# Optimization experiments

Measured on AMD Instinct MI355X. Metric: run time of the kernel, lower is better.

The kernel has to match this reference:

```python
import jax, jax.numpy as jnp
import numpy as np

V, E, H, C_TAGS, B, T = 32000, 256, 200, 20, 64, 512
LN_EPS = 1e-5


def setup_inputs() -> dict:
    key = jax.random.key(0)
    ks = jax.random.split(key, 12)
    s = 0.05
    return {
        "words": jax.random.randint(ks[0], (B, T), 0, V),
        "seq_len": jax.random.randint(ks[1], (B,), T // 2, T + 1),
        "target": jax.random.randint(ks[2], (B, T), 0, C_TAGS),
        "embed_table": jax.random.normal(ks[3], (V, E)) * s,
        "ln_gamma": jnp.ones((E,)),
        "ln_beta": jnp.zeros((E,)),
        "w_ih_f": jax.random.normal(ks[4], (4 * H, E)) * s,
        "w_hh_f": jax.random.normal(ks[5], (4 * H, H)) * s,
        "b_f": jnp.zeros((4 * H,)),  # b_ih + b_hh folded together
        "w_ih_b": jax.random.normal(ks[6], (4 * H, E)) * s,
        "w_hh_b": jax.random.normal(ks[7], (4 * H, H)) * s,
        "b_b": jnp.zeros((4 * H,)),
        "fc_w": jax.random.normal(ks[8], (C_TAGS, 2 * H)) * s,
        "fc_b": jnp.zeros((C_TAGS,)),
        "trans": jax.random.normal(ks[9], (C_TAGS, C_TAGS)) * s,
        "start_scores": jax.random.normal(ks[10], (C_TAGS,)) * s,
        "end_scores": jax.random.normal(ks[11], (C_TAGS,)) * s,
    }


def _lstm_dir(x, m, w_ih, w_hh, b, reverse):
    """x: [T,B,E] time-major, m: [T,B] float mask. Packed-sequence semantics:
    carry only updates on valid steps (matters for the reverse direction)."""
    Hn = w_hh.shape[1]
    gates_x = jnp.einsum('tbe,ge->tbg', x, w_ih) + b  # [T,B,4H], batched GEMM

    def step(carry, xs):
        h, c = carry
        gx, mt = xs
        g = gx + h @ w_hh.T
        i, f, gg, o = jnp.split(g, 4, axis=-1)  # torch gate order i,f,g,o
        c_new = jax.nn.sigmoid(f) * c + jax.nn.sigmoid(i) * jnp.tanh(gg)
        h_new = jax.nn.sigmoid(o) * jnp.tanh(c_new)
        mt = mt[:, None]
        h = mt * h_new + (1.0 - mt) * h
        c = mt * c_new + (1.0 - mt) * c
        return (h, c), h

    init = (jnp.zeros((x.shape[1], Hn), x.dtype), jnp.zeros((x.shape[1], Hn), x.dtype))
    _, hs = jax.lax.scan(step, init, (gates_x, m), reverse=reverse)
    return hs  # [T,B,H]


def _crf_nll(logits, mask, target, trans, start, end):
    """Linear-chain CRF NLL with start/end transitions. logits [B,T,C] (emissions),
    mask [B,T] float, target [B,T] int. Returns per-sample loss [B]."""
    # --- log partition via forward algorithm (scan over time) ---
    alpha0 = start[None, :] + logits[:, 0]  # [B,C]
    emits = jnp.swapaxes(logits, 0, 1)[1:]  # [T-1,B,C]
    ms = jnp.swapaxes(mask, 0, 1)[1:]       # [T-1,B]

    def step(alpha, xs):
        emit, mt = xs
        scores = alpha[:, :, None] + trans[None, :, :] + emit[:, None, :]  # [B,C,C]
        new = jax.nn.logsumexp(scores, axis=1)
        alpha = jnp.where(mt[:, None] > 0, new, alpha)
        return alpha, None

    alpha, _ = jax.lax.scan(step, alpha0, (emits, ms))
    logZ = jax.nn.logsumexp(alpha + end[None, :], axis=1)  # [B]

    # --- gold path score ---
    emit_gold = jnp.take_along_axis(logits, target[..., None], axis=2)[..., 0]  # [B,T]
    emit_score = jnp.sum(emit_gold * mask, axis=1)
    trans_gold = trans[target[:, :-1], target[:, 1:]]  # [B,T-1]
    trans_score = jnp.sum(trans_gold * mask[:, 1:], axis=1)
    last_idx = jnp.sum(mask, axis=1).astype(jnp.int32) - 1
    last_tag = jnp.take_along_axis(target, last_idx[:, None], axis=1)[:, 0]
    gold = emit_score + trans_score + start[target[:, 0]] + end[last_tag]
    return logZ - gold


def reference(words, seq_len, target, embed_table, ln_gamma, ln_beta,
              w_ih_f, w_hh_f, b_f, w_ih_b, w_hh_b, b_b,
              fc_w, fc_b, trans, start_scores, end_scores):
    # Embedding + LayerNorm
    x = embed_table[words]  # [B,T,E]
    mu = x.mean(-1, keepdims=True)
    var = ((x - mu) ** 2).mean(-1, keepdims=True)
    x = (x - mu) * jax.lax.rsqrt(var + LN_EPS) * ln_gamma + ln_beta

    mask = (jnp.arange(x.shape[1])[None, :] < seq_len[:, None]).astype(x.dtype)  # [B,T]
    xt = jnp.swapaxes(x, 0, 1)       # [T,B,E]
    mt = jnp.swapaxes(mask, 0, 1)    # [T,B]

    # BiLSTM (num_layers=1)
    hf = _lstm_dir(xt, mt, w_ih_f, w_hh_f, b_f, reverse=False)
    hb = _lstm_dir(xt, mt, w_ih_b, w_hh_b, b_b, reverse=True)
    feats = jnp.swapaxes(jnp.concatenate([hf, hb], axis=-1), 0, 1)  # [B,T,2H]

    # fc + dropout (eval: identity) + log_softmax emissions
    feats = feats @ fc_w.T + fc_b
    logits = jax.nn.log_softmax(feats, axis=-1)

    loss = _crf_nll(logits, mask, target, trans, start_scores, end_scores)
    return loss.mean()
```

## Files before the change

### kernel.cpp

```cpp
#include <hip/hip_runtime.h>

#define TT 512
#define BB 64
#define EE 256
#define HH 200
#define GG 800
#define CC 20
#define MM (BB * TT)

typedef _Float16 f16x8 __attribute__((ext_vector_type(8)));
typedef float    f32x4 __attribute__((ext_vector_type(4)));
typedef _Float16 f16x2 __attribute__((ext_vector_type(2)));

#if __has_builtin(__builtin_amdgcn_mfma_f32_16x16x32_f16)
#define HAVE_MFMA_F16 1
#else
#define HAVE_MFMA_F16 0
#endif

__device__ __forceinline__ float bf2f(unsigned short u) {
  return __uint_as_float(((unsigned int)u) << 16);
}
__device__ __forceinline__ unsigned short f2bf(float f) {
  unsigned int u = __float_as_uint(f);
  return (unsigned short)((u + 0x7fffu + ((u >> 16) & 1u)) >> 16);
}
__device__ __forceinline__ float sigf(float x) { return 1.0f / (1.0f + __expf(-x)); }
__device__ __forceinline__ float tanhfast(float x) {
  return 1.0f - 2.0f / (__expf(2.0f * x) + 1.0f);
}
union U32H2 { unsigned int u; f16x2 h; };
__device__ __forceinline__ unsigned int bfpair_to_h2bits(unsigned int p) {
  U32H2 r;
  r.h[0] = (_Float16)bf2f((unsigned short)(p & 0xffffu));
  r.h[1] = (_Float16)bf2f((unsigned short)(p >> 16));
  return r.u;
}
__device__ __forceinline__ float dot2acc(f16x2 a, f16x2 b, float c) {
#if __has_builtin(__builtin_amdgcn_fdot2)
  return __builtin_amdgcn_fdot2(a, b, c, false);
#else
  return c + (float)a[0] * (float)b[0] + (float)a[1] * (float)b[1];
#endif
}

#define NSEG 14
struct CvtArgs { const void* src[NSEG]; };
__constant__ const int cvt_cum[NSEG + 1] = {
    0, 8192000, 8192256, 8192512, 8397312, 8557312, 8558112,
    8762912, 8922912, 8923712, 8931712, 8931732, 8932132, 8932152, 8932172};

__global__ __launch_bounds__(256) void k_convert(CvtArgs a,
                                                 unsigned short* __restrict__ dst) {
  const bool f32mode = (((const unsigned int*)a.src[1])[0] == 0x3F800000u);
  int gi0 = (blockIdx.x * 256 + threadIdx.x) * 4;
#pragma unroll
  for (int r = 0; r < 4; ++r) {
    int gi = gi0 + r;
    if (gi >= cvt_cum[NSEG]) return;
    int seg = 0;
#pragma unroll
    for (int s = 1; s < NSEG; ++s) seg += (gi >= cvt_cum[s]) ? 1 : 0;
    int local = gi - cvt_cum[seg];
    unsigned short v;
    if (f32mode) v = f2bf(((const float*)a.src[seg])[local]);
    else         v = ((const unsigned short*)a.src[seg])[local];
    dst[gi] = v;
  }
}

__global__ __launch_bounds__(256) void k_embed_ln(
    const int* __restrict__ words, const unsigned short* __restrict__ etab,
    const unsigned short* __restrict__ gamma, const unsigned short* __restrict__ beta,
    unsigned short* __restrict__ x) {
  int m = blockIdx.x;
  int e = threadIdx.x;
  int w = words[m];
  float v = bf2f(etab[(size_t)w * EE + e]);
  float s = v, ss = v * v;
#pragma unroll
  for (int off = 32; off > 0; off >>= 1) {
    s += __shfl_xor(s, off, 64);
    ss += __shfl_xor(ss, off, 64);
  }
  __shared__ float red[2][4];
  int wv = e >> 6;
  if ((e & 63) == 0) { red[0][wv] = s; red[1][wv] = ss; }
  __syncthreads();
  float S = red[0][0] + red[0][1] + red[0][2] + red[0][3];
  float SS = red[1][0] + red[1][1] + red[1][2] + red[1][3];
  float mu = S * (1.0f / EE);
  float var = fmaxf(SS * (1.0f / EE) - mu * mu, 0.0f);
  float nrm = (v - mu) * rsqrtf(var + 1e-5f) * bf2f(gamma[e]) + bf2f(beta[e]);
  x[(size_t)m * EE + e] = f2bf(nrm);
}

#if HAVE_MFMA_F16
__global__ __launch_bounds__(256) void k_gates(
    const unsigned short* __restrict__ x,
    const unsigned short* __restrict__ wih_f, const unsigned short* __restrict__ wih_b,
    const unsigned short* __restrict__ bias_f, const unsigned short* __restrict__ bias_b,
    unsigned short* __restrict__ gates) {
  const int dir = blockIdx.z;
  const unsigned short* wih = dir ? wih_b : wih_f;
  const unsigned short* bias = dir ? bias_b : bias_f;
  const int m0 = blockIdx.x * 64;
  const int n0 = blockIdx.y * 64;
  __shared__ __align__(16) _Float16 As[64 * 32];
  __shared__ __align__(16) _Float16 Bs[64 * 32];
  const int tid = threadIdx.x;
  const int lane = tid & 63, wave = tid >> 6;
  const int wm = (wave >> 1) * 32, wn = (wave & 1) * 32;
  const int srow = tid >> 2, sq = tid & 3;
  const int mrow = lane & 15, q = lane >> 4;
  f32x4 acc[2][2] = {};
  for (int kk = 0; kk < EE; kk += 32) {
    union { int4 v; unsigned short u[8]; } ua, ub;
    ua.v = *(const int4*)(x + (size_t)(m0 + srow) * EE + kk + sq * 8);
    ub.v.x = 0; ub.v.y = 0; ub.v.z = 0; ub.v.w = 0;
    int n = n0 + srow;
    if (n < GG) ub.v = *(const int4*)(wih + (size_t)n * EE + kk + sq * 8);
    f16x8 af, bf;
#pragma unroll
    for (int r = 0; r < 8; ++r) {
      af[r] = (_Float16)bf2f(ua.u[r]);
      bf[r] = (_Float16)bf2f(ub.u[r]);
    }
    __syncthreads();
    *(f16x8*)(As + srow * 32 + sq * 8) = af;
    *(f16x8*)(Bs + srow * 32 + sq * 8) = bf;
    __syncthreads();
    f16x8 a0 = *(const f16x8*)(As + (wm + mrow) * 32 + q * 8);
    f16x8 a1 = *(const f16x8*)(As + (wm + 16 + mrow) * 32 + q * 8);
    f16x8 b0 = *(const f16x8*)(Bs + (wn + mrow) * 32 + q * 8);
    f16x8 b1 = *(const f16x8*)(Bs + (wn + 16 + mrow) * 32 + q * 8);
    acc[0][0] = __builtin_amdgcn_mfma_f32_16x16x32_f16(a0, b0, acc[0][0], 0, 0, 0);
    acc[0][1] = __builtin_amdgcn_mfma_f32_16x16x32_f16(a0, b1, acc[0][1], 0, 0, 0);
    acc[1][0] = __builtin_amdgcn_mfma_f32_16x16x32_f16(a1, b0, acc[1][0], 0, 0, 0);
    acc[1][1] = __builtin_amdgcn_mfma_f32_16x16x32_f16(a1, b1, acc[1][1], 0, 0, 0);
  }
#pragma unroll
  for (int im = 0; im < 2; ++im) {
#pragma unroll
    for (int in = 0; in < 2; ++in) {
      int n = n0 + wn + in * 16 + mrow;
      if (n < GG) {
        float bb = bf2f(bias[n]);
#pragma unroll
        for (int r = 0; r < 4; ++r) {
          int mg = m0 + wm + im * 16 + q * 4 + r;
          gates[((size_t)dir * MM + mg) * GG + n] = f2bf(acc[im][in][r] + bb);
        }
      }
    }
  }
}
#else
__global__ __launch_bounds__(256) void k_gates(
    const unsigned short* __restrict__ x,
    const unsigned short* __restrict__ wih_f, const unsigned short* __restrict__ wih_b,
    const unsigned short* __restrict__ bias_f, const unsigned short* __restrict__ bias_b,
    unsigned short* __restrict__ gates) {
  const int dir = blockIdx.z;
  const unsigned short* wih = dir ? wih_b : wih_f;
  const unsigned short* bias = dir ? bias_b : bias_f;
  const int m0 = blockIdx.x * 64;
  const int n0 = blockIdx.y * 64;
  for (int r = 0; r < 16; ++r) {
    int idx = threadIdx.x + 256 * r;
    int m = m0 + (idx >> 6), n = n0 + (idx & 63);
    if (n >= GG) continue;
    float acc = bf2f(bias[n]);
    const unsigned short* xr = x + (size_t)m * EE;
    const unsigned short* wr = wih + (size_t)n * EE;
    for (int k = 0; k < EE; ++k) acc += bf2f(xr[k]) * bf2f(wr[k]);
    gates[((size_t)dir * MM + m) * GG + n] = f2bf(acc);
  }
}
#endif

__global__ __launch_bounds__(832)
__attribute__((amdgpu_waves_per_eu(4, 4)))
void k_lstm(
    const unsigned short* __restrict__ gates,
    const unsigned short* __restrict__ whh_f, const unsigned short* __restrict__ whh_b,
    const int* __restrict__ seq_len,
    unsigned short* __restrict__ h_out) {
  const int b = blockIdx.x & (BB - 1);
  const int dir = blockIdx.x >> 6;
  const unsigned short* whh = dir ? whh_b : whh_f;
  const int tid = threadIdx.x;
  const int L = seq_len[b];
  __shared__ __align__(16) _Float16 hsh[HH];
  __shared__ float gbuf[GG];
  unsigned int w2u[100];
  if (tid < GG) {
    const unsigned short* wr = whh + (size_t)tid * HH;
#pragma unroll
    for (int i = 0; i < 25; ++i) {
      int4 wvv = *(const int4*)(wr + i * 8);
      w2u[4 * i + 0] = bfpair_to_h2bits((unsigned int)wvv.x);
      w2u[4 * i + 1] = bfpair_to_h2bits((unsigned int)wvv.y);
      w2u[4 * i + 2] = bfpair_to_h2bits((unsigned int)wvv.z);
      w2u[4 * i + 3] = bfpair_to_h2bits((unsigned int)wvv.w);
      asm volatile("" : "+v"(w2u[4 * i + 0]), "+v"(w2u[4 * i + 1]),
                        "+v"(w2u[4 * i + 2]), "+v"(w2u[4 * i + 3]));
    }
  }
  if (tid < HH) hsh[tid] = (_Float16)0.0f;
  float c_st = 0.0f, h_st = 0.0f;
  const unsigned short* gbase = gates + ((size_t)dir * MM + (size_t)b * TT) * GG + tid;
  unsigned short* hobase = h_out + (size_t)(dir * BB + b) * TT * HH;
  float gx_cur = 0.0f;
  if (tid < GG) {
    int t0 = dir ? (TT - 1) : 0;
    gx_cur = bf2f(gbase[(size_t)t0 * GG]);
  }
  __syncthreads();
  for (int s = 0; s < TT; ++s) {
    const int t = dir ? (TT - 1 - s) : s;
    if (tid < GG) {
      int sn = (s + 1 < TT) ? (s + 1) : s;
      int tn = dir ? (TT - 1 - sn) : sn;
      float gx_next = bf2f(gbase[(size_t)tn * GG]);
      float acc0 = gx_cur, acc1 = 0.0f;
#pragma unroll
      for (int g = 0; g < 7; ++g) {
        const int nk = (g < 6) ? 4 : 1;
        union { int4 v; f16x2 h[4]; } u[4];
#pragma unroll
        for (int k = 0; k < 4; ++k)
          if (k < nk) u[k].v = *(const int4*)(hsh + (g * 4 + k) * 8);
#pragma unroll
        for (int k = 0; k < 4; ++k) {
          if (k < nk) {
            const int i = g * 4 + k;
            U32H2 w0, w1, w2, w3;
            w0.u = w2u[4 * i + 0]; w1.u = w2u[4 * i + 1];
            w2.u = w2u[4 * i + 2]; w3.u = w2u[4 * i + 3];
            acc0 = dot2acc(w0.h, u[k].h[0], acc0);
            acc1 = dot2acc(w1.h, u[k].h[1], acc1);
            acc0 = dot2acc(w2.h, u[k].h[2], acc0);
            acc1 = dot2acc(w3.h, u[k].h[3], acc1);
          }
        }
#if __has_builtin(__builtin_amdgcn_sched_barrier)
        __builtin_amdgcn_sched_barrier(0);
#endif
      }
      gbuf[tid] = acc0 + acc1;
      gx_cur = gx_next;
    }
    __syncthreads();
    if (tid < HH) {
      float gi = gbuf[tid], gf = gbuf[HH + tid];
      float gg = gbuf[2 * HH + tid], go = gbuf[3 * HH + tid];
      float cn = sigf(gf) * c_st + sigf(gi) * tanhfast(gg);
      float hn = sigf(go) * tanhfast(cn);
      if (t < L) { c_st = cn; h_st = hn; }
      hsh[tid] = (_Float16)h_st;
      hobase[(size_t)t * HH + tid] = f2bf(h_st);
    }
    __syncthreads();
  }
}

__global__ __launch_bounds__(256) void k_fc(
    const unsigned short* __restrict__ h_out,
    const unsigned short* __restrict__ fc_w, const unsigned short* __restrict__ fc_b,
    float* __restrict__ logits) {
  __shared__ __align__(16) unsigned short hsh[4][2 * HH];
  const int wv = threadIdx.x >> 6, lane = threadIdx.x & 63;
  const int m = blockIdx.x * 4 + wv;
  if (lane < 25) {
    *(int4*)&hsh[wv][lane * 8] = *(const int4*)(h_out + (size_t)m * HH + lane * 8);
  } else if (lane < 50) {
    *(int4*)&hsh[wv][HH + (lane - 25) * 8] =
        *(const int4*)(h_out + (size_t)MM * HH + (size_t)m * HH + (lane - 25) * 8);
  }
  __syncthreads();
  float s = -3.0e38f;
  if (lane < CC) {
    s = bf2f(fc_b[lane]);
    const unsigned short* wrow = fc_w + lane * 2 * HH;
    for (int jj = 0; jj < 50; ++jj) {
      union { int4 v; unsigned short u[8]; } hw, ww;
      hw.v = *(const int4*)&hsh[wv][jj * 8];
      ww.v = *(const int4*)(wrow + jj * 8);
#pragma unroll
      for (int r = 0; r < 8; ++r) s += bf2f(hw.u[r]) * bf2f(ww.u[r]);
    }
  }
  float mx = s;
#pragma unroll
  for (int off = 32; off > 0; off >>= 1) mx = fmaxf(mx, __shfl_xor(mx, off, 64));
  float ex = (lane < CC) ? __expf(s - mx) : 0.0f;
  float sm = ex;
#pragma unroll
  for (int off = 32; off > 0; off >>= 1) sm += __shfl_xor(sm, off, 64);
  if (lane < CC) logits[(size_t)m * CC + lane] = s - mx - __logf(sm);
}

__global__ __launch_bounds__(64) void k_crf(
    const float* __restrict__ logits, const int* __restrict__ target,
    const int* __restrict__ seq_len, const unsigned short* __restrict__ trans,
    const unsigned short* __restrict__ startv, const unsigned short* __restrict__ endv,
    float* __restrict__ loss_b) {
  const int b = blockIdx.x, lane = threadIdx.x;
  const int L = seq_len[b];
  const int* tg = target + b * TT;
  const float* lg = logits + (size_t)b * TT * CC;
  float tcol[CC];
#pragma unroll
  for (int i = 0; i < CC; ++i) tcol[i] = (lane < CC) ? bf2f(trans[i * CC + lane]) : 0.0f;
  float g = 0.0f;
  for (int t = lane; t < TT; t += 64) {
    if (t < L) {
      g += lg[t * CC + tg[t]];
      if (t >= 1) g += bf2f(trans[tg[t - 1] * CC + tg[t]]);
    }
  }
#pragma unroll
  for (int off = 32; off > 0; off >>= 1) g += __shfl_xor(g, off, 64);
  float alpha = (lane < CC) ? (bf2f(startv[lane]) + lg[lane]) : -3.0e38f;
  for (int t = 1; t < L; ++t) {
    float e = (lane < CC) ? lg[t * CC + lane] : 0.0f;
    float sc[CC];
#pragma unroll
    for (int i = 0; i < CC; ++i) sc[i] = __shfl(alpha, i, 64) + tcol[i];
    float mx = sc[0];
#pragma unroll
    for (int i = 1; i < CC; ++i) mx = fmaxf(mx, sc[i]);
    float sm = 0.0f;
#pragma unroll
    for (int i = 0; i < CC; ++i) sm += __expf(sc[i] - mx);
    float na = mx + __logf(sm) + e;
    if (lane < CC) alpha = na;
  }
  float v = (lane < CC) ? (alpha + bf2f(endv[lane])) : -3.0e38f;
  float mx = v;
#pragma unroll
  for (int off = 32; off > 0; off >>= 1) mx = fmaxf(mx, __shfl_xor(mx, off, 64));
  float ex = (lane < CC) ? __expf(v - mx) : 0.0f;
#pragma unroll
  for (int off = 32; off > 0; off >>= 1) ex += __shfl_xor(ex, off, 64);
  if (lane == 0) {
    float logZ = mx + __logf(ex);
    float gold = g + bf2f(startv[tg[0]]) + bf2f(endv[tg[L - 1]]);
    loss_b[b] = logZ - gold;
  }
}

__global__ __launch_bounds__(64) void k_mean(const float* __restrict__ loss_b,
                                             unsigned int* __restrict__ out) {
  float v = loss_b[threadIdx.x];
#pragma unroll
  for (int off = 32; off > 0; off >>= 1) v += __shfl_xor(v, off, 64);
  if (threadIdx.x == 0) {
    float mean = v * (1.0f / BB);
    unsigned int lo = (unsigned int)f2bf(mean);
    unsigned int hi = __float_as_uint(mean) >> 16;
    out[0] = (hi << 16) | lo;
  }
}

extern "C" void kernel_launch(void* const* d_in, const int* in_sizes, int n_in,
                              void* d_out, int out_size, void* d_ws, size_t ws_size,
                              hipStream_t stream) {
  const int* words   = (const int*)d_in[0];
  const int* seq_len = (const int*)d_in[1];
  const int* target  = (const int*)d_in[2];

  char* ws = (char*)d_ws;
  const size_t x_off      = 0;
  const size_t gates_off  = x_off + 16777216;
  const size_t h_off      = gates_off + 104857600;
  const size_t logits_off = h_off + 26214400;
  const size_t loss_off   = logits_off + 2621440;
  const size_t cvt_off    = loss_off + 256;
  unsigned short* x      = (unsigned short*)(ws + x_off);
  unsigned short* gatesb = (unsigned short*)(ws + gates_off);
  unsigned short* h_out  = (unsigned short*)(ws + h_off);
  float* logits          = (float*)(ws + logits_off);
  float* loss_b          = (float*)(ws + loss_off);
  unsigned short* wcvt   = (unsigned short*)(ws + cvt_off);

  unsigned short* etab_c  = wcvt + 0;
  unsigned short* gamma_c = wcvt + 8192000;
  unsigned short* beta_c  = wcvt + 8192256;
  unsigned short* wih_f_c = wcvt + 8192512;
  unsigned short* whh_f_c = wcvt + 8397312;
  unsigned short* b_f_c   = wcvt + 8557312;
  unsigned short* wih_b_c = wcvt + 8558112;
  unsigned short* whh_b_c = wcvt + 8762912;
  unsigned short* b_b_c   = wcvt + 8922912;
  unsigned short* fc_w_c  = wcvt + 8923712;
  unsigned short* fc_b_c  = wcvt + 8931712;
  unsigned short* trans_c = wcvt + 8931732;
  unsigned short* start_c = wcvt + 8932132;
  unsigned short* end_c   = wcvt + 8932152;

  CvtArgs ca;
  for (int i = 0; i < NSEG; ++i) ca.src[i] = d_in[3 + i];
  const int total_cvt = 8932172;
  k_convert<<<(total_cvt + 1023) / 1024, 256, 0, stream>>>(ca, wcvt);

  k_embed_ln<<<MM, 256, 0, stream>>>(words, etab_c, gamma_c, beta_c, x);
  k_gates<<<dim3(MM / 64, 13, 2), 256, 0, stream>>>(x, wih_f_c, wih_b_c, b_f_c, b_b_c, gatesb);
  k_lstm<<<128, 832, 0, stream>>>(gatesb, whh_f_c, whh_b_c, seq_len, h_out);
  k_fc<<<MM / 4, 256, 0, stream>>>(h_out, fc_w_c, fc_b_c, logits);
  k_crf<<<BB, 64, 0, stream>>>(logits, target, seq_len, trans_c, start_c, end_c, loss_b);
  k_mean<<<1, 64, 0, stream>>>(loss_b, (unsigned int*)d_out);
}
```

Before: 1.199 ms.

## Compute all four gates per thread in LSTM recurrence, double-buffer hidden state

The recurrent LSTM kernel now runs one thread per hidden unit instead of one thread per gate row. Each thread holds the four gate rows of W_hh in registers (400 packed half2 words) and computes the gate pre-activations and the cell update itself. This removes the shared gate buffer and one of the two barriers per timestep. The hidden state in shared memory is double-buffered to avoid a read/write race. The cost is serial work per thread growing about fourfold, and a very large register footprint at one wave per EU, which risks spilling and lower latency hiding.

```diff
diff --git a/kernel.cpp b/kernel.cpp
--- a/kernel.cpp
+++ b/kernel.cpp
@@ -179,8 +179,8 @@
 }
 #endif
 
-__global__ __launch_bounds__(832)
-__attribute__((amdgpu_waves_per_eu(4, 4)))
+__global__ __launch_bounds__(256)
+__attribute__((amdgpu_waves_per_eu(1, 1)))
 void k_lstm(
     const unsigned short* __restrict__ gates,
     const unsigned short* __restrict__ whh_f, const unsigned short* __restrict__ whh_b,
@@ -191,75 +191,81 @@
   const unsigned short* whh = dir ? whh_b : whh_f;
   const int tid = threadIdx.x;
   const int L = seq_len[b];
-  __shared__ __align__(16) _Float16 hsh[HH];
-  __shared__ float gbuf[GG];
-  unsigned int w2u[100];
-  if (tid < GG) {
-    const unsigned short* wr = whh + (size_t)tid * HH;
-#pragma unroll
-    for (int i = 0; i < 25; ++i) {
-      int4 wvv = *(const int4*)(wr + i * 8);
-      w2u[4 * i + 0] = bfpair_to_h2bits((unsigned int)wvv.x);
-      w2u[4 * i + 1] = bfpair_to_h2bits((unsigned int)wvv.y);
-      w2u[4 * i + 2] = bfpair_to_h2bits((unsigned int)wvv.z);
-      w2u[4 * i + 3] = bfpair_to_h2bits((unsigned int)wvv.w);
-      asm volatile("" : "+v"(w2u[4 * i + 0]), "+v"(w2u[4 * i + 1]),
-                        "+v"(w2u[4 * i + 2]), "+v"(w2u[4 * i + 3]));
-    }
-  }
-  if (tid < HH) hsh[tid] = (_Float16)0.0f;
+  __shared__ __align__(16) _Float16 hsh[2][HH];
+  unsigned int w2u[400];
+  if (tid < HH) {
+#pragma unroll
+    for (int r = 0; r < 4; ++r) {
+      const unsigned short* wr = whh + (size_t)(tid + r * HH) * HH;
+#pragma unroll
+      for (int i = 0; i < 25; ++i) {
+        int4 wv = *(const int4*)(wr + i * 8);
+        const int base = r * 100 + i * 4;
+        w2u[base + 0] = bfpair_to_h2bits((unsigned int)wv.x);
+        w2u[base + 1] = bfpair_to_h2bits((unsigned int)wv.y);
+        w2u[base + 2] = bfpair_to_h2bits((unsigned int)wv.z);
+        w2u[base + 3] = bfpair_to_h2bits((unsigned int)wv.w);
+        asm volatile("" : "+v"(w2u[base + 0]), "+v"(w2u[base + 1]),
+                          "+v"(w2u[base + 2]), "+v"(w2u[base + 3]));
+      }
+    }
+    hsh[0][tid] = (_Float16)0.0f;
+  }
   float c_st = 0.0f, h_st = 0.0f;
-  const unsigned short* gbase = gates + ((size_t)dir * MM + (size_t)b * TT) * GG + tid;
+  const unsigned short* gbase = gates + ((size_t)dir * MM + (size_t)b * TT) * GG;
   unsigned short* hobase = h_out + (size_t)(dir * BB + b) * TT * HH;
-  float gx_cur = 0.0f;
-  if (tid < GG) {
-    int t0 = dir ? (TT - 1) : 0;
-    gx_cur = bf2f(gbase[(size_t)t0 * GG]);
+  float gx0 = 0, gx1 = 0, gx2 = 0, gx3 = 0;
+  if (tid < HH) {
+    const int t0 = dir ? (TT - 1) : 0;
+    gx0 = bf2f(gbase[(size_t)t0 * GG + tid]);
+    gx1 = bf2f(gbase[(size_t)t0 * GG + tid + HH]);
+    gx2 = bf2f(gbase[(size_t)t0 * GG + tid + 2 * HH]);
+    gx3 = bf2f(gbase[(size_t)t0 * GG + tid + 3 * HH]);
   }
   __syncthreads();
   for (int s = 0; s < TT; ++s) {
     const int t = dir ? (TT - 1 - s) : s;
-    if (tid < GG) {
-      int sn = (s + 1 < TT) ? (s + 1) : s;
-      int tn = dir ? (TT - 1 - sn) : sn;
-      float gx_next = bf2f(gbase[(size_t)tn * GG]);
-      float acc0 = gx_cur, acc1 = 0.0f;
-#pragma unroll
-      for (int g = 0; g < 7; ++g) {
-        const int nk = (g < 6) ? 4 : 1;
-        union { int4 v; f16x2 h[4]; } u[4];
-#pragma unroll
-        for (int k = 0; k < 4; ++k)
-          if (k < nk) u[k].v = *(const int4*)(hsh + (g * 4 + k) * 8);
-#pragma unroll
-        for (int k = 0; k < 4; ++k) {
-          if (k < nk) {
-            const int i = g * 4 + k;
+    const int p = s & 1;
+    if (tid < HH) {
+      const int sn = (s + 1 < TT) ? (s + 1) : s;
+      const int tn = dir ? (TT - 1 - sn) : sn;
+      float n0 = bf2f(gbase[(size_t)tn * GG + tid]);
+      float n1 = bf2f(gbase[(size_t)tn * GG + tid + HH]);
+      float n2 = bf2f(gbase[(size_t)tn * GG + tid + 2 * HH]);
+      float n3 = bf2f(gbase[(size_t)tn * GG + tid + 3 * HH]);
+      float a0 = gx0, a1 = gx1, a2 = gx2, a3 = gx3;
+#pragma unroll
+      for (int grp = 0; grp < 5; ++grp) {
+        union { int4 v; f16x2 h[4]; } u[5];
+#pragma unroll
+        for (int k = 0; k < 5; ++k)
+          u[k].v = *(const int4*)(&hsh[p][0] + (grp * 5 + k) * 8);
+#pragma unroll
+        for (int k = 0; k < 5; ++k) {
+          const int cw = (grp * 5 + k) * 4;
+#pragma unroll
+          for (int j = 0; j < 4; ++j) {
             U32H2 w0, w1, w2, w3;
-            w0.u = w2u[4 * i + 0]; w1.u = w2u[4 * i + 1];
-            w2.u = w2u[4 * i + 2]; w3.u = w2u[4 * i + 3];
-            acc0 = dot2acc(w0.h, u[k].h[0], acc0);
-            acc1 = dot2acc(w1.h, u[k].h[1], acc1);
-            acc0 = dot2acc(w2.h, u[k].h[2], acc0);
-            acc1 = dot2acc(w3.h, u[k].h[3], acc1);
+            w0.u = w2u[0 * 100 + cw + j];
+            w1.u = w2u[1 * 100 + cw + j];
+            w2.u = w2u[2 * 100 + cw + j];
+            w3.u = w2u[3 * 100 + cw + j];
+            a0 = dot2acc(w0.h, u[k].h[j], a0);
+            a1 = dot2acc(w1.h, u[k].h[j], a1);
+            a2 = dot2acc(w2.h, u[k].h[j], a2);
+            a3 = dot2acc(w3.h, u[k].h[j], a3);
           }
         }
 #if __has_builtin(__builtin_amdgcn_sched_barrier)
         __builtin_amdgcn_sched_barrier(0);
 #endif
       }
-      gbuf[tid] = acc0 + acc1;
-      gx_cur = gx_next;
-    }
-    __syncthreads();
-    if (tid < HH) {
-      float gi = gbuf[tid], gf = gbuf[HH + tid];
-      float gg = gbuf[2 * HH + tid], go = gbuf[3 * HH + tid];
-      float cn = sigf(gf) * c_st + sigf(gi) * tanhfast(gg);
-      float hn = sigf(go) * tanhfast(cn);
+      float cn = sigf(a1) * c_st + sigf(a0) * tanhfast(a2);
+      float hn = sigf(a3) * tanhfast(cn);
       if (t < L) { c_st = cn; h_st = hn; }
-      hsh[tid] = (_Float16)h_st;
+      hsh[p ^ 1][tid] = (_Float16)h_st;
       hobase[(size_t)t * HH + tid] = f2bf(h_st);
+      gx0 = n0; gx1 = n1; gx2 = n2; gx3 = n3;
     }
     __syncthreads();
   }
@@ -407,7 +413,7 @@
 
   k_embed_ln<<<MM, 256, 0, stream>>>(words, etab_c, gamma_c, beta_c, x);
   k_gates<<<dim3(MM / 64, 13, 2), 256, 0, stream>>>(x, wih_f_c, wih_b_c, b_f_c, b_b_c, gatesb);
-  k_lstm<<<128, 832, 0, stream>>>(gatesb, whh_f_c, whh_b_c, seq_len, h_out);
+  k_lstm<<<128, 256, 0, stream>>>(gatesb, whh_f_c, whh_b_c, seq_len, h_out);
   k_fc<<<MM / 4, 256, 0, stream>>>(h_out, fc_w_c, fc_b_c, logits);
   k_crf<<<BB, 64, 0, stream>>>(logits, target, seq_len, trans_c, start_c, end_c, loss_b);
   k_mean<<<1, 64, 0, stream>>>(loss_b, (unsigned int*)d_out);
```

Measured after the change: 1.329 ms. 10.9% more time.
